# Kernel optimization log

Measured on AMD Instinct MI355X. Metric: run time of the kernel, lower is better.

Reference implementation:

```python
import jax, jax.numpy as jnp
import numpy as np

N_A, N_P, E, H, L = 50000, 100000, 500000, 256, 3


def setup_inputs() -> dict:
    key = jax.random.key(0)
    ks = jax.random.split(key, 8)

    def edges(k, n_src, n_dst):
        k1, k2 = jax.random.split(k)
        src = jax.random.randint(k1, (E,), 0, n_src, dtype=jnp.int64 if jax.config.jax_enable_x64 else jnp.int32)
        dst = jax.random.randint(k2, (E,), 0, n_dst, dtype=src.dtype)
        return jnp.stack([src, dst])  # [2, E]

    scale = 1.0 / np.sqrt(H).astype(np.float32)
    return {
        "x_author": jax.random.normal(ks[0], (N_A, H), jnp.float32),
        "x_paper": jax.random.normal(ks[1], (N_P, H), jnp.float32),
        "edge_writes": edges(ks[2], N_A, N_P),   # author -> paper
        "edge_rev": edges(ks[3], N_P, N_A),      # paper  -> author
        "edge_cites": edges(ks[4], N_P, N_P),    # paper  -> paper
        # per-layer, per-edge-type SAGEConv params: [L, n_edge_types=3, ...]
        "Wl": jax.random.normal(ks[5], (L, 3, H, H), jnp.float32) * scale,  # neighbor lin (with bias)
        "bl": jnp.zeros((L, 3, H), jnp.float32),
        "Wr": jax.random.normal(ks[6], (L, 3, H, H), jnp.float32) * scale,  # root lin (no bias)
    }


def _sage(x_src, x_dst, edge, Wl, bl, Wr):
    # SAGEConv: lin_l(mean_{j->i} x_src[j]) + lin_r(x_dst)
    src, dst = edge[0], edge[1]
    n_dst = x_dst.shape[0]
    msum = jax.ops.segment_sum(x_src[src], dst, num_segments=n_dst)        # [n_dst, H]
    cnt = jax.ops.segment_sum(jnp.ones(src.shape, x_src.dtype), dst, num_segments=n_dst)
    mean = msum / jnp.maximum(cnt, 1.0)[:, None]  # nodes with no in-edges stay 0
    return mean @ Wl + bl + x_dst @ Wr


def reference(x_author, x_paper, edge_writes, edge_rev, edge_cites, Wl, bl, Wr):
    xa, xp = x_author, x_paper
    for l in range(L):  # fixed small layer loop
        # HeteroConv aggr='sum' over edge types sharing dst node type
        out_p = _sage(xa, xp, edge_writes, Wl[l, 0], bl[l, 0], Wr[l, 0]) \
              + _sage(xp, xp, edge_cites, Wl[l, 2], bl[l, 2], Wr[l, 2])
        out_a = _sage(xp, xa, edge_rev, Wl[l, 1], bl[l, 1], Wr[l, 1])
        xa, xp = out_a, out_p
    return xa, xp
```

## Files before the change

### kernel.cpp

```cpp
#include <hip/hip_runtime.h>
#include <hip/hip_bf16.h>
#include <cstdint>
#include <cstddef>

#define NA 50000
#define NP 100000
#define HH 256
#define LL 3
#define GP8 12500
#define GA8 6250

typedef __attribute__((ext_vector_type(8))) short short8;
typedef __attribute__((ext_vector_type(4))) float f32x4;

__device__ __forceinline__ float bf2f(unsigned int u16) {
    unsigned int x = u16 << 16;
    return __builtin_bit_cast(float, x);
}
__device__ __forceinline__ unsigned short f2bf(float f) {
    __hip_bfloat16 h = __float2bfloat16(f);
    return __builtin_bit_cast(unsigned short, h);
}

__global__ void prep_w_k(const float* __restrict__ Wl, const float* __restrict__ Wr,
                         unsigned short* __restrict__ WT) {
    int gid = blockIdx.x * 256 + threadIdx.x;
    int w = gid >> 16;
    int within = gid & 65535;
    int n = within >> 8, k = within & 255;
    int l = w / 5, t = w % 5;
    float v;
    if (t == 0)      v = Wl[(size_t)((l * 3 + 0) * 256 + k) * 256 + n];
    else if (t == 1) v = Wl[(size_t)((l * 3 + 2) * 256 + k) * 256 + n];
    else if (t == 2) v = Wr[(size_t)((l * 3 + 0) * 256 + k) * 256 + n] +
                         Wr[(size_t)((l * 3 + 2) * 256 + k) * 256 + n];
    else if (t == 3) v = Wl[(size_t)((l * 3 + 1) * 256 + k) * 256 + n];
    else             v = Wr[(size_t)((l * 3 + 1) * 256 + k) * 256 + n];
    int h = n >> 7, nl = n & 127;
    int lb = nl * 512 + (k << 1);
    int swz = lb ^ ((nl & 7) << 4);
    *reinterpret_cast<unsigned short*>(
        reinterpret_cast<char*>(WT) + (size_t)w * 131072 + (size_t)h * 65536 + swz) = f2bf(v);
}

__global__ void prep_bias_k(const float* __restrict__ bl,
                            float* __restrict__ biasP, float* __restrict__ biasA) {
    int gid = blockIdx.x * 256 + threadIdx.x;
    int l = gid >> 8, n = gid & 255;
    biasP[l * 256 + n] = bl[(l * 3 + 0) * 256 + n] + bl[(l * 3 + 2) * 256 + n];
    biasA[l * 256 + n] = bl[(l * 3 + 1) * 256 + n];
}

__global__ void count3_k(const int* __restrict__ dw, const int* __restrict__ dc,
                         const int* __restrict__ dr, int* __restrict__ cnt,
                         int E, int egrid) {
    int b = blockIdx.x;
    int type = b / egrid, lb = b - type * egrid;
    int e = lb * 256 + threadIdx.x;
    if (e >= E) return;
    const int* d = (type == 0) ? dw : (type == 1) ? dc : dr;
    int base = (type == 0) ? 0 : (type == 1) ? NP : 2 * NP;
    atomicAdd(&cnt[base + d[e]], 1);
}

__global__ void scanA_k(const int* __restrict__ cnt, int* __restrict__ part,
                        int nbP, int nbA) {
    int b = blockIdx.x;
    int type, lb;
    if (b < nbP) { type = 0; lb = b; }
    else if (b < 2 * nbP) { type = 1; lb = b - nbP; }
    else { type = 2; lb = b - 2 * nbP; }
    int n = (type < 2) ? NP : NA;
    int base = (type == 0) ? 0 : (type == 1) ? NP : 2 * NP;
    __shared__ int sh[256];
    int i = lb * 256 + threadIdx.x;
    sh[threadIdx.x] = (i < n) ? cnt[base + i] : 0;
    __syncthreads();
    for (int s = 128; s > 0; s >>= 1) {
        if (threadIdx.x < s) sh[threadIdx.x] += sh[threadIdx.x + s];
        __syncthreads();
    }
    if (threadIdx.x == 0) part[type * 512 + lb] = sh[0];
}
__global__ void scanB_k(int* __restrict__ part, int nbP, int nbA) {
    int type = blockIdx.x;
    int nb = (type < 2) ? nbP : nbA;
    int* seg = part + type * 512;
    __shared__ int sh[512];
    int t = threadIdx.x;
    int v0 = (t < nb) ? seg[t] : 0;
    sh[t] = v0;
    __syncthreads();
    for (int off = 1; off < 512; off <<= 1) {
        int x = (t >= off) ? sh[t - off] : 0;
        __syncthreads();
        sh[t] += x;
        __syncthreads();
    }
    if (t < nb) seg[t] = sh[t] - v0;
}
__global__ void scanC_k(const int* __restrict__ cnt, const int* __restrict__ part,
                        int* __restrict__ rp_w, int* __restrict__ rp_c,
                        int* __restrict__ rp_r, int nbP, int nbA) {
    int b = blockIdx.x;
    int type, lb;
    if (b < nbP) { type = 0; lb = b; }
    else if (b < 2 * nbP) { type = 1; lb = b - nbP; }
    else { type = 2; lb = b - 2 * nbP; }
    int n = (type < 2) ? NP : NA;
    int base = (type == 0) ? 0 : (type == 1) ? NP : 2 * NP;
    int* rowptr = (type == 0) ? rp_w : (type == 1) ? rp_c : rp_r;
    __shared__ int sh[256];
    int t = threadIdx.x;
    int i = lb * 256 + t;
    int v = (i < n) ? cnt[base + i] : 0;
    sh[t] = v;
    __syncthreads();
    for (int off = 1; off < 256; off <<= 1) {
        int x = (t >= off) ? sh[t - off] : 0;
        __syncthreads();
        if (t >= off) sh[t] += x;
        __syncthreads();
    }
    if (i < n) {
        int incl = sh[t];
        int pb = part[type * 512 + lb];
        rowptr[i] = pb + incl - v;
        if (i == n - 1) rowptr[n] = pb + incl;
    }
}
__global__ void fill3_k(const int* __restrict__ e_w, const int* __restrict__ e_c,
                        const int* __restrict__ e_r,
                        const int* __restrict__ rp_w, const int* __restrict__ rp_c,
                        const int* __restrict__ rp_r,
                        int* __restrict__ cursor,
                        int* __restrict__ col_w, int* __restrict__ col_c,
                        int* __restrict__ col_r, int E, int egrid) {
    int b = blockIdx.x;
    int type = b / egrid, lb = b - type * egrid;
    int e = lb * 256 + threadIdx.x;
    if (e >= E) return;
    const int* ep = (type == 0) ? e_w : (type == 1) ? e_c : e_r;
    const int* rowptr = (type == 0) ? rp_w : (type == 1) ? rp_c : rp_r;
    int* col = (type == 0) ? col_w : (type == 1) ? col_c : col_r;
    int base = (type == 0) ? 0 : (type == 1) ? NP : 2 * NP;
    int s = ep[e], d = ep[E + e];
    int pos = atomicAdd(&cursor[base + d], 1);
    col[rowptr[d] + pos] = s;
}

__global__ void cast_bf16_k(const float* __restrict__ x, unsigned short* __restrict__ o, int n8) {
    int g = blockIdx.x * 256 + threadIdx.x;
    if (g >= n8) return;
    const float4* xp = reinterpret_cast<const float4*>(x) + (size_t)g * 2;
    float4 a = xp[0], b = xp[1];
    union { unsigned short u[8]; uint4 v; } r;
    r.u[0] = f2bf(a.x); r.u[1] = f2bf(a.y); r.u[2] = f2bf(a.z); r.u[3] = f2bf(a.w);
    r.u[4] = f2bf(b.x); r.u[5] = f2bf(b.y); r.u[6] = f2bf(b.z); r.u[7] = f2bf(b.w);
    reinterpret_cast<uint4*>(o)[g] = r.v;
}

__global__ void agg_fused_k(const unsigned short* __restrict__ xa,
                            const unsigned short* __restrict__ xp,
                            const int* __restrict__ rp_w, const int* __restrict__ col_w,
                            const int* __restrict__ rp_c, const int* __restrict__ col_c,
                            const int* __restrict__ rp_r, const int* __restrict__ col_r,
                            unsigned short* __restrict__ mW,
                            unsigned short* __restrict__ mC,
                            unsigned short* __restrict__ mR) {
    int b = blockIdx.x;
    const unsigned short* x; const int* rp; const int* cl; unsigned short* mn; int nd;
    if (b < GP8)            { x = xa; rp = rp_w; cl = col_w; mn = mW; nd = NP; }
    else if (b < 2 * GP8)   { b -= GP8; x = xp; rp = rp_c; cl = col_c; mn = mC; nd = NP; }
    else                    { b -= 2 * GP8; x = xp; rp = rp_r; cl = col_r; mn = mR; nd = NA; }
    int node = b * 8 + (threadIdx.x >> 5);
    if (node >= nd) return;
    const int l32 = threadIdx.x & 31;
    int beg = rp[node], end = rp[node + 1];
    int deg = end - beg;
    float a0 = 0.f, a1 = 0.f, a2 = 0.f, a3 = 0.f, a4 = 0.f, a5 = 0.f, a6 = 0.f, a7 = 0.f;
    for (int base = 0; base < deg; base += 32) {
        int n = min(deg - base, 32);
        int myc = (base + l32 < deg) ? cl[beg + base + l32] : 0;
        int i = 0;
        for (; i + 1 < n; i += 2) {
            int s0 = __shfl(myc, i, 32);
            int s1 = __shfl(myc, i + 1, 32);
            uint4 v0 = *reinterpret_cast<const uint4*>(x + (size_t)s0 * 256 + l32 * 8);
            uint4 v1 = *reinterpret_cast<const uint4*>(x + (size_t)s1 * 256 + l32 * 8);
            a0 += bf2f(v0.x & 0xffffu); a1 += bf2f(v0.x >> 16);
            a2 += bf2f(v0.y & 0xffffu); a3 += bf2f(v0.y >> 16);
            a4 += bf2f(v0.z & 0xffffu); a5 += bf2f(v0.z >> 16);
            a6 += bf2f(v0.w & 0xffffu); a7 += bf2f(v0.w >> 16);
            a0 += bf2f(v1.x & 0xffffu); a1 += bf2f(v1.x >> 16);
            a2 += bf2f(v1.y & 0xffffu); a3 += bf2f(v1.y >> 16);
            a4 += bf2f(v1.z & 0xffffu); a5 += bf2f(v1.z >> 16);
            a6 += bf2f(v1.w & 0xffffu); a7 += bf2f(v1.w >> 16);
        }
        if (i < n) {
            int s0 = __shfl(myc, i, 32);
            uint4 v0 = *reinterpret_cast<const uint4*>(x + (size_t)s0 * 256 + l32 * 8);
            a0 += bf2f(v0.x & 0xffffu); a1 += bf2f(v0.x >> 16);
            a2 += bf2f(v0.y & 0xffffu); a3 += bf2f(v0.y >> 16);
            a4 += bf2f(v0.z & 0xffffu); a5 += bf2f(v0.z >> 16);
            a6 += bf2f(v0.w & 0xffffu); a7 += bf2f(v0.w >> 16);
        }
    }
    float sc = (deg > 0) ? 1.0f / (float)deg : 0.f;
    uint4 r;
    r.x = (unsigned int)f2bf(a0 * sc) | ((unsigned int)f2bf(a1 * sc) << 16);
    r.y = (unsigned int)f2bf(a2 * sc) | ((unsigned int)f2bf(a3 * sc) << 16);
    r.z = (unsigned int)f2bf(a4 * sc) | ((unsigned int)f2bf(a5 * sc) << 16);
    r.w = (unsigned int)f2bf(a6 * sc) | ((unsigned int)f2bf(a7 * sc) << 16);
    *reinterpret_cast<uint4*>(mn + (size_t)node * 256 + l32 * 8) = r;
}

#define EP_STRIDE 132
template <bool LAST>
__global__ __launch_bounds__(512, 2)
void gemm_fat_k(const unsigned short* __restrict__ mW, const unsigned short* __restrict__ mC,
                const unsigned short* __restrict__ xp, const unsigned short* __restrict__ mR,
                const unsigned short* __restrict__ xa, const unsigned short* __restrict__ WT_l,
                const float* __restrict__ biasP, const float* __restrict__ biasA,
                void* __restrict__ outP, void* __restrict__ outA, int mtP) {
    __shared__ char lds[128 * EP_STRIDE * 4];
    char* bsh = lds;
    float* eps = reinterpret_cast<float*>(lds);
    const int tid = threadIdx.x;

    const bool isP = (int)blockIdx.x < mtP;
    const int tile = isP ? blockIdx.x : blockIdx.x - mtP;
    const int parts = isP ? 3 : 2;
    const unsigned short* A0 = isP ? mW : mR;
    const unsigned short* A1 = isP ? mC : xa;
    const unsigned short* A2 = xp;
    const char* Wb = reinterpret_cast<const char*>(isP ? WT_l : WT_l + 3 * 65536);
    const float* bias = isP ? biasP : biasA;
    void* out = isP ? outP : outA;
    const int M = isP ? NP : NA;

    const int wid = tid >> 6;
    const int l = tid & 63;
    const int rw = wid & 3, cw = wid >> 2;
    const int kgrp = (l >> 4) << 3;
    int row0 = tile * 128 + rw * 32 + (l & 15);
    int rc0 = row0 < M ? row0 : M - 1;
    int row1 = row0 + 16;
    int rc1 = row1 < M ? row1 : M - 1;

    f32x4 acc[2][8];
    #pragma unroll
    for (int h = 0; h < 2; ++h)
        #pragma unroll
        for (int t = 0; t < 8; ++t) acc[h][t] = f32x4{0.f, 0.f, 0.f, 0.f};

    bool first = true;
    for (int p = 0; p < parts; ++p) {
        const unsigned short* Ap = (p == 0) ? A0 : (p == 1) ? A1 : A2;
        uint4 af[2][8];
        const unsigned short* Ar0 = Ap + (size_t)rc0 * 256 + kgrp;
        const unsigned short* Ar1 = Ap + (size_t)rc1 * 256 + kgrp;
        #pragma unroll
        for (int s = 0; s < 8; ++s) {
            af[0][s] = *reinterpret_cast<const uint4*>(Ar0 + s * 32);
            af[1][s] = *reinterpret_cast<const uint4*>(Ar1 + s * 32);
        }

        #pragma unroll
        for (int h = 0; h < 2; ++h) {
            if (!first) __syncthreads();
            first = false;
            const char* WbH = Wb + (size_t)p * 131072 + (size_t)h * 65536;
            #pragma unroll
            for (int i = 0; i < 8; ++i) {
                __builtin_amdgcn_global_load_lds(
                    (const __attribute__((address_space(1))) unsigned int*)(WbH + (i * 512 + tid) * 16),
                    (__attribute__((address_space(3))) unsigned int*)(bsh + (i * 512 + (tid & ~63)) * 16),
                    16, 0, 0);
            }
            __syncthreads();
            #pragma unroll
            for (int s = 0; s < 8; ++s) {
                short8 a0 = __builtin_bit_cast(short8, af[0][s]);
                short8 a1 = __builtin_bit_cast(short8, af[1][s]);
                #pragma unroll
                for (int t = 0; t < 4; ++t) {
                    int n = (cw << 6) + (t << 4) + (l & 15);
                    int byte = (n * 512 + s * 64 + kgrp * 2) ^ ((n & 7) << 4);
                    short8 b = __builtin_bit_cast(short8, *reinterpret_cast<const uint4*>(bsh + byte));
                    acc[h][t]     = __builtin_amdgcn_mfma_f32_16x16x32_bf16(a0, b, acc[h][t], 0, 0, 0);
                    acc[h][4 + t] = __builtin_amdgcn_mfma_f32_16x16x32_bf16(a1, b, acc[h][4 + t], 0, 0, 0);
                }
            }
        }
    }

    const int col16 = l & 15;
    const int rq = (l >> 4) << 2;
    #pragma unroll
    for (int e = 0; e < 2; ++e) {
        __syncthreads();
        #pragma unroll
        for (int f = 0; f < 2; ++f) {
            #pragma unroll
            for (int t = 0; t < 4; ++t) {
                int lr0 = rw * 32 + f * 16 + rq;
                int lc = (cw << 6) + (t << 4) + col16;
                float badd = bias[(e << 7) + lc];
                #pragma unroll
                for (int j = 0; j < 4; ++j)
                    eps[(lr0 + j) * EP_STRIDE + lc] = acc[e][f * 4 + t][j] + badd;
            }
        }
        __syncthreads();
        if (LAST) {
            float* fout = reinterpret_cast<float*>(out);
            #pragma unroll
            for (int i = 0; i < 8; ++i) {
                int c = i * 512 + tid;
                int r = c >> 5, within = c & 31;
                int rg = tile * 128 + r;
                if (rg < M) {
                    const float* src = eps + r * EP_STRIDE + within * 4;
                    float4 v = *reinterpret_cast<const float4*>(src);
                    *reinterpret_cast<float4*>(fout + (size_t)rg * 256 + (e << 7) + within * 4) = v;
                }
            }
        } else {
            unsigned short* bout = reinterpret_cast<unsigned short*>(out);
            #pragma unroll
            for (int i = 0; i < 4; ++i) {
                int c = i * 512 + tid;
                int r = c >> 4, within = c & 15;
                int rg = tile * 128 + r;
                if (rg < M) {
                    const float* src = eps + r * EP_STRIDE + within * 8;
                    float4 lo = *reinterpret_cast<const float4*>(src);
                    float4 hi = *reinterpret_cast<const float4*>(src + 4);
                    uint4 v;
                    v.x = (unsigned int)f2bf(lo.x) | ((unsigned int)f2bf(lo.y) << 16);
                    v.y = (unsigned int)f2bf(lo.z) | ((unsigned int)f2bf(lo.w) << 16);
                    v.z = (unsigned int)f2bf(hi.x) | ((unsigned int)f2bf(hi.y) << 16);
                    v.w = (unsigned int)f2bf(hi.z) | ((unsigned int)f2bf(hi.w) << 16);
                    *reinterpret_cast<uint4*>(bout + (size_t)rg * 256 + (e << 7) + within * 8) = v;
                }
            }
        }
    }
}

extern "C" void kernel_launch(void* const* d_in, const int* in_sizes, int n_in,
                              void* d_out, int out_size, void* d_ws, size_t ws_size,
                              hipStream_t stream) {
    const float* x_author = (const float*)d_in[0];
    const float* x_paper  = (const float*)d_in[1];
    const int* e_w = (const int*)d_in[2];
    const int* e_r = (const int*)d_in[3];
    const int* e_c = (const int*)d_in[4];
    const float* Wl = (const float*)d_in[5];
    const float* bl = (const float*)d_in[6];
    const float* Wr = (const float*)d_in[7];
    const int E = in_sizes[2] / 2;

    float* outA = (float*)d_out;
    float* outP = (float*)d_out + (size_t)NA * HH;

    size_t off = 0;
    auto carve = [&](size_t bytes) {
        void* p = (char*)d_ws + off;
        off += (bytes + 255) & ~(size_t)255;
        return p;
    };
    unsigned short* xa0   = (unsigned short*)carve((size_t)NA * HH * 2);
    unsigned short* xp0   = (unsigned short*)carve((size_t)NP * HH * 2);
    unsigned short* meanW = (unsigned short*)carve((size_t)NP * HH * 2);
    unsigned short* meanC = (unsigned short*)carve((size_t)NP * HH * 2);
    unsigned short* meanR = (unsigned short*)carve((size_t)NA * HH * 2);
    unsigned short* WT    = (unsigned short*)carve((size_t)15 * 65536 * 2);
    float* biasP = (float*)carve((size_t)LL * HH * 4);
    float* biasA = (float*)carve((size_t)LL * HH * 4);
    int* cnt    = (int*)carve((size_t)(2 * NP + NA) * 4);
    int* rp_w   = (int*)carve((size_t)(NP + 1) * 4);
    int* rp_c   = (int*)carve((size_t)(NP + 1) * 4);
    int* rp_r   = (int*)carve((size_t)(NA + 1) * 4);
    int* part   = (int*)carve((size_t)2048 * 4);
    int* col_w  = (int*)carve((size_t)E * 4);
    int* col_c  = (int*)carve((size_t)E * 4);
    int* col_r  = (int*)carve((size_t)E * 4);
    (void)off; (void)ws_size; (void)n_in; (void)out_size;

    const size_t cntBytes = (size_t)(2 * NP + NA) * 4;
    const int egrid = (E + 255) / 256;
    const int nbP = (NP + 255) / 256, nbA = (NA + 255) / 256;
    const int mtP = (NP + 127) / 128, mtA = (NA + 127) / 128;

    hipMemsetAsync(cnt, 0, cntBytes, stream);
    prep_w_k<<<3840, 256, 0, stream>>>(Wl, Wr, WT);
    prep_bias_k<<<3, 256, 0, stream>>>(bl, biasP, biasA);
    count3_k<<<3 * egrid, 256, 0, stream>>>(e_w + E, e_c + E, e_r + E, cnt, E, egrid);
    scanA_k<<<2 * nbP + nbA, 256, 0, stream>>>(cnt, part, nbP, nbA);
    scanB_k<<<3, 512, 0, stream>>>(part, nbP, nbA);
    scanC_k<<<2 * nbP + nbA, 256, 0, stream>>>(cnt, part, rp_w, rp_c, rp_r, nbP, nbA);
    hipMemsetAsync(cnt, 0, cntBytes, stream);
    fill3_k<<<3 * egrid, 256, 0, stream>>>(e_w, e_c, e_r, rp_w, rp_c, rp_r,
                                           cnt, col_w, col_c, col_r, E, egrid);

    cast_bf16_k<<<(NA * HH / 8 + 255) / 256, 256, 0, stream>>>(x_author, xa0, NA * HH / 8);
    cast_bf16_k<<<(NP * HH / 8 + 255) / 256, 256, 0, stream>>>(x_paper, xp0, NP * HH / 8);

    unsigned short* xa1 = (unsigned short*)d_out;
    unsigned short* xp1 = xa1 + (size_t)NA * HH;

    unsigned short* xa_cur = xa0; unsigned short* xp_cur = xp0;
    unsigned short* xa_nxt = xa1; unsigned short* xp_nxt = xp1;

    const int aggGrid = 2 * GP8 + GA8;

    for (int l = 0; l < LL; ++l) {
        const unsigned short* WT_l = WT + (size_t)l * 5 * 65536;
        agg_fused_k<<<aggGrid, 256, 0, stream>>>(xa_cur, xp_cur, rp_w, col_w,
                                                 rp_c, col_c, rp_r, col_r,
                                                 meanW, meanC, meanR);
        if (l < LL - 1) {
            gemm_fat_k<false><<<mtP + mtA, 512, 0, stream>>>(
                meanW, meanC, xp_cur, meanR, xa_cur, WT_l,
                biasP + l * 256, biasA + l * 256, xp_nxt, xa_nxt, mtP);
            unsigned short* t;
            t = xa_cur; xa_cur = xa_nxt; xa_nxt = t;
            t = xp_cur; xp_cur = xp_nxt; xp_nxt = t;
        } else {
            gemm_fat_k<true><<<mtP + mtA, 512, 0, stream>>>(
                meanW, meanC, xp_cur, meanR, xa_cur, WT_l,
                biasP + l * 256, biasA + l * 256, outP, outA, mtP);
        }
    }
}
```

Baseline: 929.0 us.

## Retile fused SAGE GEMM to 64-row tiles split across output-column halves

The GEMM kernel moves from 128-row tiles with 512 threads covering all 256 output columns to 64-row tiles with 256 threads, one 128-column half per blockIdx.y. The K dimension is now split into two 128-wide panels. The weight layout is reordered to match, so each LDS stage holds only 32KB, and A fragments are loaded per K-panel. The aim is smaller LDS and register footprint, more blocks for occupancy and load balance, and lower epilogue LDS use. In exchange, each block re-reads its A rows for both column halves and the weight panels are loaded more times overall.

Result: slower. 952.7 us (+2.5%).

```diff
diff --git a/kernel.cpp b/kernel.cpp
--- a/kernel.cpp
+++ b/kernel.cpp
@@ -37,10 +37,12 @@
     else if (t == 3) v = Wl[(size_t)((l * 3 + 1) * 256 + k) * 256 + n];
     else             v = Wr[(size_t)((l * 3 + 1) * 256 + k) * 256 + n];
     int h = n >> 7, nl = n & 127;
-    int lb = nl * 512 + (k << 1);
+    int q = k >> 7, kl = k & 127;
+    int lb = nl * 256 + (kl << 1);
     int swz = lb ^ ((nl & 7) << 4);
     *reinterpret_cast<unsigned short*>(
-        reinterpret_cast<char*>(WT) + (size_t)w * 131072 + (size_t)h * 65536 + swz) = f2bf(v);
+        reinterpret_cast<char*>(WT) + (size_t)w * 131072 + (size_t)h * 65536 +
+        (size_t)q * 32768 + swz) = f2bf(v);
 }
 
 __global__ void prep_bias_k(const float* __restrict__ bl,
@@ -215,18 +217,17 @@
     *reinterpret_cast<uint4*>(mn + (size_t)node * 256 + l32 * 8) = r;
 }
 
-#define EP_STRIDE 132
 template <bool LAST>
-__global__ __launch_bounds__(512, 2)
+__global__ __launch_bounds__(256, 2)
 void gemm_fat_k(const unsigned short* __restrict__ mW, const unsigned short* __restrict__ mC,
                 const unsigned short* __restrict__ xp, const unsigned short* __restrict__ mR,
                 const unsigned short* __restrict__ xa, const unsigned short* __restrict__ WT_l,
                 const float* __restrict__ biasP, const float* __restrict__ biasA,
                 void* __restrict__ outP, void* __restrict__ outA, int mtP) {
-    __shared__ char lds[128 * EP_STRIDE * 4];
-    char* bsh = lds;
+    __shared__ char lds[32768];
     float* eps = reinterpret_cast<float*>(lds);
     const int tid = threadIdx.x;
+    const int h = blockIdx.y;
 
     const bool isP = (int)blockIdx.x < mtP;
     const int tile = isP ? blockIdx.x : blockIdx.x - mtP;
@@ -241,55 +242,54 @@
 
     const int wid = tid >> 6;
     const int l = tid & 63;
-    const int rw = wid & 3, cw = wid >> 2;
+    const int rw = wid & 1, cw = wid >> 1;
     const int kgrp = (l >> 4) << 3;
-    int row0 = tile * 128 + rw * 32 + (l & 15);
+    int row0 = tile * 64 + rw * 32 + (l & 15);
     int rc0 = row0 < M ? row0 : M - 1;
     int row1 = row0 + 16;
     int rc1 = row1 < M ? row1 : M - 1;
 
-    f32x4 acc[2][8];
+    f32x4 acc[2][4];
     #pragma unroll
-    for (int h = 0; h < 2; ++h)
+    for (int f = 0; f < 2; ++f)
         #pragma unroll
-        for (int t = 0; t < 8; ++t) acc[h][t] = f32x4{0.f, 0.f, 0.f, 0.f};
+        for (int t = 0; t < 4; ++t) acc[f][t] = f32x4{0.f, 0.f, 0.f, 0.f};
 
     bool first = true;
     for (int p = 0; p < parts; ++p) {
         const unsigned short* Ap = (p == 0) ? A0 : (p == 1) ? A1 : A2;
-        uint4 af[2][8];
-        const unsigned short* Ar0 = Ap + (size_t)rc0 * 256 + kgrp;
-        const unsigned short* Ar1 = Ap + (size_t)rc1 * 256 + kgrp;
         #pragma unroll
-        for (int s = 0; s < 8; ++s) {
-            af[0][s] = *reinterpret_cast<const uint4*>(Ar0 + s * 32);
-            af[1][s] = *reinterpret_cast<const uint4*>(Ar1 + s * 32);
-        }
-
-        #pragma unroll
-        for (int h = 0; h < 2; ++h) {
+        for (int q = 0; q < 2; ++q) {
             if (!first) __syncthreads();
             first = false;
-            const char* WbH = Wb + (size_t)p * 131072 + (size_t)h * 65536;
+            const char* Pan = Wb + (size_t)p * 131072 + (size_t)h * 65536 + (size_t)q * 32768;
             #pragma unroll
             for (int i = 0; i < 8; ++i) {
                 __builtin_amdgcn_global_load_lds(
-                    (const __attribute__((address_space(1))) unsigned int*)(WbH + (i * 512 + tid) * 16),
-                    (__attribute__((address_space(3))) unsigned int*)(bsh + (i * 512 + (tid & ~63)) * 16),
+                    (const __attribute__((address_space(1))) unsigned int*)(Pan + (i * 256 + tid) * 16),
+                    (__attribute__((address_space(3))) unsigned int*)(lds + (i * 256 + (tid & ~63)) * 16),
                     16, 0, 0);
+            }
+            uint4 af0[4], af1[4];
+            const unsigned short* Ar0 = Ap + (size_t)rc0 * 256 + q * 128 + kgrp;
+            const unsigned short* Ar1 = Ap + (size_t)rc1 * 256 + q * 128 + kgrp;
+            #pragma unroll
+            for (int s = 0; s < 4; ++s) {
+                af0[s] = *reinterpret_cast<const uint4*>(Ar0 + s * 32);
+                af1[s] = *reinterpret_cast<const uint4*>(Ar1 + s * 32);
             }
             __syncthreads();
             #pragma unroll
-            for (int s = 0; s < 8; ++s) {
-                short8 a0 = __builtin_bit_cast(short8, af[0][s]);
-                short8 a1 = __builtin_bit_cast(short8, af[1][s]);
+            for (int s = 0; s < 4; ++s) {
+                short8 a0 = __builtin_bit_cast(short8, af0[s]);
+                short8 a1 = __builtin_bit_cast(short8, af1[s]);
                 #pragma unroll
                 for (int t = 0; t < 4; ++t) {
                     int n = (cw << 6) + (t << 4) + (l & 15);
-                    int byte = (n * 512 + s * 64 + kgrp * 2) ^ ((n & 7) << 4);
-                    short8 b = __builtin_bit_cast(short8, *reinterpret_cast<const uint4*>(bsh + byte));
-                    acc[h][t]     = __builtin_amdgcn_mfma_f32_16x16x32_bf16(a0, b, acc[h][t], 0, 0, 0);
-                    acc[h][4 + t] = __builtin_amdgcn_mfma_f32_16x16x32_bf16(a1, b, acc[h][4 + t], 0, 0, 0);
+                    int byte = (n * 256 + s * 64 + kgrp * 2) ^ ((n & 7) << 4);
+                    short8 b = __builtin_bit_cast(short8, *reinterpret_cast<const uint4*>(lds + byte));
+                    acc[0][t] = __builtin_amdgcn_mfma_f32_16x16x32_bf16(a0, b, acc[0][t], 0, 0, 0);
+                    acc[1][t] = __builtin_amdgcn_mfma_f32_16x16x32_bf16(a1, b, acc[1][t], 0, 0, 0);
                 }
             }
         }
@@ -297,53 +297,49 @@
 
     const int col16 = l & 15;
     const int rq = (l >> 4) << 2;
+    __syncthreads();
     #pragma unroll
-    for (int e = 0; e < 2; ++e) {
-        __syncthreads();
+    for (int f = 0; f < 2; ++f) {
         #pragma unroll
-        for (int f = 0; f < 2; ++f) {
+        for (int t = 0; t < 4; ++t) {
+            int lc = (cw << 6) + (t << 4) + col16;
+            int lr0 = rw * 32 + f * 16 + rq;
+            float badd = bias[(h << 7) + lc];
             #pragma unroll
-            for (int t = 0; t < 4; ++t) {
-                int lr0 = rw * 32 + f * 16 + rq;
-                int lc = (cw << 6) + (t << 4) + col16;
-                float badd = bias[(e << 7) + lc];
-                #pragma unroll
-                for (int j = 0; j < 4; ++j)
-                    eps[(lr0 + j) * EP_STRIDE + lc] = acc[e][f * 4 + t][j] + badd;
+            for (int j = 0; j < 4; ++j)
+                eps[(lr0 + j) * 128 + lc] = acc[f][t][j] + badd;
+        }
+    }
+    __syncthreads();
+    if (LAST) {
+        float* fout = reinterpret_cast<float*>(out);
+        #pragma unroll
+        for (int i = 0; i < 8; ++i) {
+            int c = i * 256 + tid;
+            int r = c >> 5, within = c & 31;
+            int rg = tile * 64 + r;
+            if (rg < M) {
+                float4 v = *reinterpret_cast<const float4*>(eps + r * 128 + within * 4);
+                *reinterpret_cast<float4*>(fout + (size_t)rg * 256 + (h << 7) + within * 4) = v;
             }
         }
-        __syncthreads();
-        if (LAST) {
-            float* fout = reinterpret_cast<float*>(out);
-            #pragma unroll
-            for (int i = 0; i < 8; ++i) {
-                int c = i * 512 + tid;
-                int r = c >> 5, within = c & 31;
-                int rg = tile * 128 + r;
-                if (rg < M) {
-                    const float* src = eps + r * EP_STRIDE + within * 4;
-                    float4 v = *reinterpret_cast<const float4*>(src);
-                    *reinterpret_cast<float4*>(fout + (size_t)rg * 256 + (e << 7) + within * 4) = v;
-                }
-            }
-        } else {
-            unsigned short* bout = reinterpret_cast<unsigned short*>(out);
-            #pragma unroll
-            for (int i = 0; i < 4; ++i) {
-                int c = i * 512 + tid;
-                int r = c >> 4, within = c & 15;
-                int rg = tile * 128 + r;
-                if (rg < M) {
-                    const float* src = eps + r * EP_STRIDE + within * 8;
-                    float4 lo = *reinterpret_cast<const float4*>(src);
-                    float4 hi = *reinterpret_cast<const float4*>(src + 4);
-                    uint4 v;
-                    v.x = (unsigned int)f2bf(lo.x) | ((unsigned int)f2bf(lo.y) << 16);
-                    v.y = (unsigned int)f2bf(lo.z) | ((unsigned int)f2bf(lo.w) << 16);
-                    v.z = (unsigned int)f2bf(hi.x) | ((unsigned int)f2bf(hi.y) << 16);
-                    v.w = (unsigned int)f2bf(hi.z) | ((unsigned int)f2bf(hi.w) << 16);
-                    *reinterpret_cast<uint4*>(bout + (size_t)rg * 256 + (e << 7) + within * 8) = v;
-                }
+    } else {
+        unsigned short* bout = reinterpret_cast<unsigned short*>(out);
+        #pragma unroll
+        for (int i = 0; i < 4; ++i) {
+            int c = i * 256 + tid;
+            int r = c >> 4, within = c & 15;
+            int rg = tile * 64 + r;
+            if (rg < M) {
+                const float* src = eps + r * 128 + within * 8;
+                float4 lo = *reinterpret_cast<const float4*>(src);
+                float4 hi = *reinterpret_cast<const float4*>(src + 4);
+                uint4 v;
+                v.x = (unsigned int)f2bf(lo.x) | ((unsigned int)f2bf(lo.y) << 16);
+                v.y = (unsigned int)f2bf(lo.z) | ((unsigned int)f2bf(lo.w) << 16);
+                v.z = (unsigned int)f2bf(hi.x) | ((unsigned int)f2bf(hi.y) << 16);
+                v.w = (unsigned int)f2bf(hi.z) | ((unsigned int)f2bf(hi.w) << 16);
+                *reinterpret_cast<uint4*>(bout + (size_t)rg * 256 + (h << 7) + within * 8) = v;
             }
         }
     }
@@ -392,7 +388,7 @@
     const size_t cntBytes = (size_t)(2 * NP + NA) * 4;
     const int egrid = (E + 255) / 256;
     const int nbP = (NP + 255) / 256, nbA = (NA + 255) / 256;
-    const int mtP = (NP + 127) / 128, mtA = (NA + 127) / 128;
+    const int mtP = (NP + 63) / 64, mtA = (NA + 63) / 64;
 
     hipMemsetAsync(cnt, 0, cntBytes, stream);
     prep_w_k<<<3840, 256, 0, stream>>>(Wl, Wr, WT);
@@ -422,14 +418,14 @@
                                                  rp_c, col_c, rp_r, col_r,
                                                  meanW, meanC, meanR);
         if (l < LL - 1) {
-            gemm_fat_k<false><<<mtP + mtA, 512, 0, stream>>>(
+            gemm_fat_k<false><<<dim3(mtP + mtA, 2), 256, 0, stream>>>(
                 meanW, meanC, xp_cur, meanR, xa_cur, WT_l,
                 biasP + l * 256, biasA + l * 256, xp_nxt, xa_nxt, mtP);
             unsigned short* t;
             t = xa_cur; xa_cur = xa_nxt; xa_nxt = t;
             t = xp_cur; xp_cur = xp_nxt; xp_nxt = t;
         } else {
-            gemm_fat_k<true><<<mtP + mtA, 512, 0, stream>>>(
+            gemm_fat_k<true><<<dim3(mtP + mtA, 2), 256, 0, stream>>>(
                 meanW, meanC, xp_cur, meanR, xa_cur, WT_l,
                 biasP + l * 256, biasA + l * 256, outP, outA, mtP);
         }
```
